# Kernel optimization log

Measured on AMD Instinct MI355X. Metric: run time of the kernel, lower is better.

## Reference

```python
import jax, jax.numpy as jnp
import numpy as np

NEG_INF = -1e9


def setup_inputs() -> dict:
    key = jax.random.key(0)
    ks = jax.random.split(key, 6)
    B, S, ENC, DEC = 32, 2048, 1024, 1024
    decoder_hidden = jax.random.normal(ks[0], (B, DEC), dtype=jnp.float32)
    encoder_outputs = jax.random.normal(ks[1], (B, S, ENC), dtype=jnp.float32)
    mask = jax.random.randint(ks[2], (B, S), 0, 2, dtype=jnp.int32)
    # nn.Linear-style weights, scaled ~ 1/sqrt(fan_in)
    W_h = jax.random.normal(ks[3], (DEC, ENC), dtype=jnp.float32) / np.sqrt(ENC)
    W_s = jax.random.normal(ks[4], (DEC, DEC), dtype=jnp.float32) / np.sqrt(DEC)
    v = jax.random.normal(ks[5], (DEC,), dtype=jnp.float32) / np.sqrt(DEC)
    return {
        "decoder_hidden": decoder_hidden,
        "encoder_outputs": encoder_outputs,
        "mask": mask,
        "W_h": W_h,
        "W_s": W_s,
        "v": v,
    }


def reference(decoder_hidden, encoder_outputs, mask, W_h, W_s, v):
    # dec: [B, D] -> [B, 1, D]
    dec = jnp.einsum("bd,ed->be", decoder_hidden, W_s)[:, None, :]
    # enc: [B, S, E] -> [B, S, D]
    enc = jnp.einsum("bse,de->bsd", encoder_outputs, W_h)
    # energy: [B, S] via rank-1 projection with v
    energy = jnp.einsum("bsd,d->bs", jnp.tanh(enc + dec), v)
    energy = jnp.where(mask == 0, NEG_INF, energy)
    attn_weights = jax.nn.softmax(energy, axis=1)  # [B, S]
    # context: [B, E]
    context = jnp.einsum("bs,bse->be", attn_weights, encoder_outputs)
    return (context, attn_weights)
```

## Files before the change

kernel.cpp:

```cpp
#include <hip/hip_runtime.h>
#include <stdint.h>
#include <math.h>

typedef __attribute__((ext_vector_type(8))) short short8;
typedef __attribute__((ext_vector_type(4))) float f32x4;

#define S_LEN 2048
#define NBATCH 32
#define KDIM 1024
#define NEG_INF_F (-1e9f)

#define BM 256
#define BN 256

__device__ __forceinline__ uint32_t pack_bf16(float f0, float f1) {
    union { float f; uint32_t u; } a, b; a.f = f0; b.f = f1;
    return ((a.u + 0x8000u) >> 16) | ((b.u + 0x8000u) & 0xFFFF0000u);
}

__device__ __forceinline__ void gload_lds16(const unsigned short* g, unsigned short* l) {
    __builtin_amdgcn_global_load_lds(
        (const __attribute__((address_space(1))) void*)g,
        (__attribute__((address_space(3))) void*)l, 16, 0, 0);
}

__device__ __forceinline__ float fast_tanh(float x) {
    float e = __expf(2.0f * x);
    return 1.0f - 2.0f * __builtin_amdgcn_rcpf(e + 1.0f);
}

__global__ __launch_bounds__(256) void dec_kernel(
    const float* __restrict__ dh, const float* __restrict__ Ws,
    float* __restrict__ dec)
{
    __shared__ float wrow[1024];
    int e = blockIdx.x;
    int t = threadIdx.x;
    #pragma unroll
    for (int i = t; i < 1024; i += 256) wrow[i] = Ws[(size_t)e * 1024 + i];
    __syncthreads();
    int b = t >> 3, part = t & 7;
    const float* dhp = dh + (size_t)b * 1024 + part * 128;
    const float* wp  = wrow + part * 128;
    float s = 0.f;
    #pragma unroll 8
    for (int i = 0; i < 128; ++i) s += dhp[i] * wp[i];
    s += __shfl_xor(s, 1);
    s += __shfl_xor(s, 2);
    s += __shfl_xor(s, 4);
    if (part == 0) dec[(size_t)b * 1024 + e] = s;
}

__global__ __launch_bounds__(256) void convert_frag_B(
    const float* __restrict__ src, unsigned short* __restrict__ out)
{
    int gid = blockIdx.x * 4 + (threadIdx.x >> 6);
    int lane = threadIdx.x & 63;
    int ms = gid & 63, ks = gid >> 6;
    const float* p = src + (size_t)(ms * 16 + (lane & 15)) * 1024
                         + ks * 32 + (lane >> 4) * 8;
    f32x4 a = *(const f32x4*)p;
    f32x4 b = *(const f32x4*)(p + 4);
    union { uint32_t d[4]; short8 v; } o;
    o.d[0] = pack_bf16(a.x, a.y); o.d[1] = pack_bf16(a.z, a.w);
    o.d[2] = pack_bf16(b.x, b.y); o.d[3] = pack_bf16(b.z, b.w);
    *(short8*)(out + (size_t)gid * 512 + lane * 8) = o.v;
}

__global__ __launch_bounds__(512, 2) void energy_gemm_v11(
    const float* __restrict__ x,
    const unsigned short* __restrict__ Bhi,
    const float* __restrict__ dec, const float* __restrict__ v,
    float* __restrict__ energy)
{
    __shared__ unsigned short lds[65536];

    int bid = blockIdx.x;
    int lid = (bid & 7) * 128 + (bid >> 3);
    int mblk = lid >> 2, nblk = lid & 3;
    int m0 = mblk * BM, n0 = nblk * BN;
    int b = m0 >> 11;

    int t = threadIdx.x, wid = t >> 6, lane = t & 63;
    int wm = wid >> 2, wn = wid & 3;
    int kg = lane >> 4, lr = lane & 15;

    f32x4 acc[8][4] = {};

    int arow = t >> 1, acg = t & 1;
    const float* aptr = x + (size_t)(m0 + arow) * KDIM + acg * 16;
    int awbase = arow * 64;
    int ax = (arow & 7) << 3;

    int rx = (lr & 7) << 3;

    f32x4 A0, A1, A2, A3;

    auto stageB = [&](int t2, unsigned short* bufB) {
        #pragma unroll
        for (int i = 0; i < 4; ++i) {
            int c = wid * 4 + i;
            int ks = 2 * t2 + (c >> 4);
            gload_lds16(Bhi + ((size_t)ks * 64 + nblk * 16 + (c & 15)) * 512 + lane * 8,
                        &bufB[c * 512]);
        }
    };

#define A_LOAD(t2, bb) { \
    const float* ap_ = aptr + (t2) * 64 + (bb) * 32; \
    A0 = *(const f32x4*)ap_;        A1 = *(const f32x4*)(ap_ + 4); \
    A2 = *(const f32x4*)(ap_ + 8);  A3 = *(const f32x4*)(ap_ + 12); }
#define A_WRITE(bufA, bb) { \
    union { uint32_t d[8]; } o_; \
    o_.d[0] = pack_bf16(A0.x, A0.y); o_.d[1] = pack_bf16(A0.z, A0.w); \
    o_.d[2] = pack_bf16(A1.x, A1.y); o_.d[3] = pack_bf16(A1.z, A1.w); \
    o_.d[4] = pack_bf16(A2.x, A2.y); o_.d[5] = pack_bf16(A2.z, A2.w); \
    o_.d[6] = pack_bf16(A3.x, A3.y); o_.d[7] = pack_bf16(A3.z, A3.w); \
    int c8_ = ((bb) * 4 + acg * 2) * 8; \
    *(short8*)&(bufA)[awbase + (c8_ ^ ax)]       = *(short8*)&o_.d[0]; \
    *(short8*)&(bufA)[awbase + ((c8_ + 8) ^ ax)] = *(short8*)&o_.d[4]; }

#define KSLOT(bufA, bufB, ksl) { \
    short8 bf[4]; \
    _Pragma("unroll") \
    for (int ni = 0; ni < 4; ++ni) \
        bf[ni] = *(const short8*)&(bufB)[((ksl) * 16 + wn * 4 + ni) * 512 + lane * 8]; \
    _Pragma("unroll") \
    for (int mi = 0; mi < 8; ++mi) { \
        short8 af = *(const short8*)&(bufA)[(wm * 128 + mi * 16 + lr) * 64 \
                        + ((((ksl) * 4 + kg) * 8) ^ rx)]; \
        _Pragma("unroll") \
        for (int ni = 0; ni < 4; ++ni) \
            acc[mi][ni] = __builtin_amdgcn_mfma_f32_16x16x32_bf16(af, bf[ni], acc[mi][ni], 0, 0, 0); \
    } }

    {
        unsigned short* bufA = &lds[0];
        stageB(0, &lds[16384]);
        A_LOAD(0, 0); A_WRITE(bufA, 0);
        A_LOAD(0, 1); A_WRITE(bufA, 1);
    }
    asm volatile("s_waitcnt vmcnt(0) lgkmcnt(0)" ::: "memory");
    __builtin_amdgcn_s_barrier();

    for (int ts = 0; ts < 16; ++ts) {
        unsigned short* bufA = &lds[(ts & 1) * 32768];
        unsigned short* bufB = bufA + 16384;
        unsigned short* nbufA = &lds[((ts + 1) & 1) * 32768];
        unsigned short* nbufB = nbufA + 16384;
        const bool st = (ts < 15);

        if (st) {
            stageB(ts + 1, nbufB);
            A_LOAD(ts + 1, 0);
            KSLOT(bufA, bufB, 0);
            A_WRITE(nbufA, 0);
            __builtin_amdgcn_sched_barrier(0);
            A_LOAD(ts + 1, 1);
            KSLOT(bufA, bufB, 1);
            A_WRITE(nbufA, 1);
        } else {
            KSLOT(bufA, bufB, 0);
            KSLOT(bufA, bufB, 1);
        }

        asm volatile("s_waitcnt vmcnt(0) lgkmcnt(0)" ::: "memory");
        __builtin_amdgcn_s_barrier();
    }

    float vv[4], dd[4];
    #pragma unroll
    for (int ni = 0; ni < 4; ++ni) {
        int d = n0 + wn * 64 + ni * 16 + lr;
        vv[ni] = v[d];
        dd[ni] = dec[(size_t)b * 1024 + d];
    }
    #pragma unroll
    for (int mi = 0; mi < 8; ++mi) {
        #pragma unroll
        for (int r = 0; r < 4; ++r) {
            float local = 0.f;
            #pragma unroll
            for (int ni = 0; ni < 4; ++ni)
                local += fast_tanh(acc[mi][ni][r] + dd[ni]) * vv[ni];
            local += __shfl_xor(local, 1);
            local += __shfl_xor(local, 2);
            local += __shfl_xor(local, 4);
            local += __shfl_xor(local, 8);
            if (lr == 0) {
                int m = m0 + wm * 128 + mi * 16 + kg * 4 + r;
                atomicAdd(&energy[m], local);
            }
        }
    }
}

__global__ __launch_bounds__(256) void softmax_kernel(
    const float* __restrict__ energy, const int* __restrict__ mask,
    float* __restrict__ attn)
{
    int b = blockIdx.x;
    int t = threadIdx.x;
    int wid = t >> 6, lane = t & 63;
    __shared__ float wmax[4], wsum[4];

    float vals[8];
    float mx = -INFINITY;
    #pragma unroll
    for (int j = 0; j < 8; ++j) {
        int s = t + j * 256;
        float e = energy[(size_t)b * S_LEN + s];
        if (mask[(size_t)b * S_LEN + s] == 0) e = NEG_INF_F;
        vals[j] = e;
        mx = fmaxf(mx, e);
    }
    #pragma unroll
    for (int m = 1; m < 64; m <<= 1) mx = fmaxf(mx, __shfl_xor(mx, m));
    if (lane == 0) wmax[wid] = mx;
    __syncthreads();
    mx = fmaxf(fmaxf(wmax[0], wmax[1]), fmaxf(wmax[2], wmax[3]));

    float sum = 0.f;
    #pragma unroll
    for (int j = 0; j < 8; ++j) { vals[j] = expf(vals[j] - mx); sum += vals[j]; }
    #pragma unroll
    for (int m = 1; m < 64; m <<= 1) sum += __shfl_xor(sum, m);
    if (lane == 0) wsum[wid] = sum;
    __syncthreads();
    sum = wsum[0] + wsum[1] + wsum[2] + wsum[3];
    float inv = 1.f / sum;
    #pragma unroll
    for (int j = 0; j < 8; ++j)
        attn[(size_t)b * S_LEN + t + j * 256] = vals[j] * inv;
}

__global__ __launch_bounds__(256) void context_kernel(
    const float* __restrict__ attn, const float* __restrict__ x,
    float* __restrict__ ctx)
{
    int ec = blockIdx.x, b = blockIdx.y, sc = blockIdx.z;
    int e = ec * 256 + threadIdx.x;
    const float* xp = x + ((size_t)b * S_LEN + sc * 128) * KDIM + e;
    const float* ap = attn + (size_t)b * S_LEN + sc * 128;
    float acc = 0.f;
    #pragma unroll 4
    for (int s = 0; s < 128; ++s) acc += ap[s] * xp[(size_t)s * KDIM];
    atomicAdd(&ctx[(size_t)b * KDIM + e], acc);
}

extern "C" void kernel_launch(void* const* d_in, const int* in_sizes, int n_in,
                              void* d_out, int out_size, void* d_ws, size_t ws_size,
                              hipStream_t stream) {
    const float* dh   = (const float*)d_in[0];
    const float* x    = (const float*)d_in[1];
    const int*   mask = (const int*)d_in[2];
    const float* Wh   = (const float*)d_in[3];
    const float* Ws   = (const float*)d_in[4];
    const float* v    = (const float*)d_in[5];

    float* ctx  = (float*)d_out;
    float* attn = (float*)d_out + 32 * 1024;

    unsigned short* Bhi = (unsigned short*)d_ws;
    float* dec    = (float*)(Bhi + 1048576ull);
    float* energy = dec + 32768;

    hipMemsetAsync(energy, 0, 65536 * sizeof(float), stream);
    hipMemsetAsync(ctx, 0, 32768 * sizeof(float), stream);

    dec_kernel<<<1024, 256, 0, stream>>>(dh, Ws, dec);
    convert_frag_B<<<512, 256, 0, stream>>>(Wh, Bhi);
    energy_gemm_v11<<<1024, 512, 0, stream>>>(x, Bhi, dec, v, energy);
    softmax_kernel<<<NBATCH, 256, 0, stream>>>(energy, mask, attn);
    context_kernel<<<dim3(4, NBATCH, 16), 256, 0, stream>>>(attn, x, ctx);
}
```

Measured before the change: 268.1 us.

## Switch energy GEMM to 32x32x16 bf16 MFMA with matching B fragment layout

Replaces the 16x16x32 MFMA tiling with 32x32x16 bf16 MFMAs. Each wave now holds 4x2 f32x16 accumulators, and the weight pre-conversion kernel and the B staging are re-laid out for 32-wide fragments. The larger instruction raises math per LDS fragment load, which cuts LDS read traffic per FLOP. In exchange the epilogue row mapping gets more complex and needs one extra shuffle-reduce step.

```diff
diff --git a/kernel.cpp b/kernel.cpp
--- a/kernel.cpp
+++ b/kernel.cpp
@@ -4,6 +4,7 @@
 
 typedef __attribute__((ext_vector_type(8))) short short8;
 typedef __attribute__((ext_vector_type(4))) float f32x4;
+typedef __attribute__((ext_vector_type(16))) float f32x16;
 
 #define S_LEN 2048
 #define NBATCH 32
@@ -51,14 +52,14 @@
     if (part == 0) dec[(size_t)b * 1024 + e] = s;
 }
 
-__global__ __launch_bounds__(256) void convert_frag_B(
+__global__ __launch_bounds__(256) void convert_frag_B32(
     const float* __restrict__ src, unsigned short* __restrict__ out)
 {
     int gid = blockIdx.x * 4 + (threadIdx.x >> 6);
     int lane = threadIdx.x & 63;
-    int ms = gid & 63, ks = gid >> 6;
-    const float* p = src + (size_t)(ms * 16 + (lane & 15)) * 1024
-                         + ks * 32 + (lane >> 4) * 8;
+    int ns = gid & 31, ks = gid >> 5;
+    const float* p = src + (size_t)(ns * 32 + (lane & 31)) * 1024
+                         + ks * 16 + (lane >> 5) * 8;
     f32x4 a = *(const f32x4*)p;
     f32x4 b = *(const f32x4*)(p + 4);
     union { uint32_t d[4]; short8 v; } o;
@@ -67,7 +68,7 @@
     *(short8*)(out + (size_t)gid * 512 + lane * 8) = o.v;
 }
 
-__global__ __launch_bounds__(512, 2) void energy_gemm_v11(
+__global__ __launch_bounds__(512, 2) void energy_gemm_v12(
     const float* __restrict__ x,
     const unsigned short* __restrict__ Bhi,
     const float* __restrict__ dec, const float* __restrict__ v,
@@ -83,16 +84,15 @@
 
     int t = threadIdx.x, wid = t >> 6, lane = t & 63;
     int wm = wid >> 2, wn = wid & 3;
-    int kg = lane >> 4, lr = lane & 15;
-
-    f32x4 acc[8][4] = {};
+    int l31 = lane & 31, l5 = lane >> 5;
+
+    f32x16 acc[4][2] = {};
 
     int arow = t >> 1, acg = t & 1;
     const float* aptr = x + (size_t)(m0 + arow) * KDIM + acg * 16;
     int awbase = arow * 64;
     int ax = (arow & 7) << 3;
-
-    int rx = (lr & 7) << 3;
+    int rx = (lane & 7) << 3;
 
     f32x4 A0, A1, A2, A3;
 
@@ -100,8 +100,9 @@
         #pragma unroll
         for (int i = 0; i < 4; ++i) {
             int c = wid * 4 + i;
-            int ks = 2 * t2 + (c >> 4);
-            gload_lds16(Bhi + ((size_t)ks * 64 + nblk * 16 + (c & 15)) * 512 + lane * 8,
+            int ks = t2 * 4 + (c >> 3);
+            int ns = nblk * 8 + (c & 7);
+            gload_lds16(Bhi + ((size_t)ks * 32 + ns) * 512 + lane * 8,
                         &bufB[c * 512]);
         }
     };
@@ -121,17 +122,14 @@
     *(short8*)&(bufA)[awbase + ((c8_ + 8) ^ ax)] = *(short8*)&o_.d[4]; }
 
 #define KSLOT(bufA, bufB, ksl) { \
-    short8 bf[4]; \
+    short8 bf0 = *(const short8*)&(bufB)[((ksl) * 8 + wn * 2 + 0) * 512 + lane * 8]; \
+    short8 bf1 = *(const short8*)&(bufB)[((ksl) * 8 + wn * 2 + 1) * 512 + lane * 8]; \
     _Pragma("unroll") \
-    for (int ni = 0; ni < 4; ++ni) \
-        bf[ni] = *(const short8*)&(bufB)[((ksl) * 16 + wn * 4 + ni) * 512 + lane * 8]; \
-    _Pragma("unroll") \
-    for (int mi = 0; mi < 8; ++mi) { \
-        short8 af = *(const short8*)&(bufA)[(wm * 128 + mi * 16 + lr) * 64 \
-                        + ((((ksl) * 4 + kg) * 8) ^ rx)]; \
-        _Pragma("unroll") \
-        for (int ni = 0; ni < 4; ++ni) \
-            acc[mi][ni] = __builtin_amdgcn_mfma_f32_16x16x32_bf16(af, bf[ni], acc[mi][ni], 0, 0, 0); \
+    for (int mf = 0; mf < 4; ++mf) { \
+        short8 af = *(const short8*)&(bufA)[(wm * 128 + mf * 32 + l31) * 64 \
+                        + ((((ksl) * 2 + l5) * 8) ^ rx)]; \
+        acc[mf][0] = __builtin_amdgcn_mfma_f32_32x32x16_bf16(af, bf0, acc[mf][0], 0, 0, 0); \
+        acc[mf][1] = __builtin_amdgcn_mfma_f32_32x32x16_bf16(af, bf1, acc[mf][1], 0, 0, 0); \
     } }
 
     {
@@ -154,41 +152,44 @@
             stageB(ts + 1, nbufB);
             A_LOAD(ts + 1, 0);
             KSLOT(bufA, bufB, 0);
+            KSLOT(bufA, bufB, 1);
             A_WRITE(nbufA, 0);
             __builtin_amdgcn_sched_barrier(0);
             A_LOAD(ts + 1, 1);
-            KSLOT(bufA, bufB, 1);
+            KSLOT(bufA, bufB, 2);
+            KSLOT(bufA, bufB, 3);
             A_WRITE(nbufA, 1);
         } else {
             KSLOT(bufA, bufB, 0);
             KSLOT(bufA, bufB, 1);
+            KSLOT(bufA, bufB, 2);
+            KSLOT(bufA, bufB, 3);
         }
 
         asm volatile("s_waitcnt vmcnt(0) lgkmcnt(0)" ::: "memory");
         __builtin_amdgcn_s_barrier();
     }
 
-    float vv[4], dd[4];
-    #pragma unroll
-    for (int ni = 0; ni < 4; ++ni) {
-        int d = n0 + wn * 64 + ni * 16 + lr;
-        vv[ni] = v[d];
-        dd[ni] = dec[(size_t)b * 1024 + d];
-    }
-    #pragma unroll
-    for (int mi = 0; mi < 8; ++mi) {
+    float vv[2], dd[2];
+    #pragma unroll
+    for (int nf = 0; nf < 2; ++nf) {
+        int d = n0 + wn * 64 + nf * 32 + l31;
+        vv[nf] = v[d];
+        dd[nf] = dec[(size_t)b * 1024 + d];
+    }
+    #pragma unroll
+    for (int mf = 0; mf < 4; ++mf) {
         #pragma unroll
-        for (int r = 0; r < 4; ++r) {
-            float local = 0.f;
-            #pragma unroll
-            for (int ni = 0; ni < 4; ++ni)
-                local += fast_tanh(acc[mi][ni][r] + dd[ni]) * vv[ni];
+        for (int r = 0; r < 16; ++r) {
+            float local = fast_tanh(acc[mf][0][r] + dd[0]) * vv[0]
+                        + fast_tanh(acc[mf][1][r] + dd[1]) * vv[1];
             local += __shfl_xor(local, 1);
             local += __shfl_xor(local, 2);
             local += __shfl_xor(local, 4);
             local += __shfl_xor(local, 8);
-            if (lr == 0) {
-                int m = m0 + wm * 128 + mi * 16 + kg * 4 + r;
+            local += __shfl_xor(local, 16);
+            if (l31 == 0) {
+                int m = m0 + wm * 128 + mf * 32 + (r & 3) + 8 * (r >> 2) + 4 * l5;
                 atomicAdd(&energy[m], local);
             }
         }
@@ -269,8 +270,8 @@
     hipMemsetAsync(ctx, 0, 32768 * sizeof(float), stream);
 
     dec_kernel<<<1024, 256, 0, stream>>>(dh, Ws, dec);
-    convert_frag_B<<<512, 256, 0, stream>>>(Wh, Bhi);
-    energy_gemm_v11<<<1024, 512, 0, stream>>>(x, Bhi, dec, v, energy);
+    convert_frag_B32<<<512, 256, 0, stream>>>(Wh, Bhi);
+    energy_gemm_v12<<<1024, 512, 0, stream>>>(x, Bhi, dec, v, energy);
     softmax_kernel<<<NBATCH, 256, 0, stream>>>(energy, mask, attn);
     context_kernel<<<dim3(4, NBATCH, 16), 256, 0, stream>>>(attn, x, ctx);
 }
```

Measured after the change: 337.0 us. 1.26x slower.
